# Optimization experiments

Hardware: AMD Instinct MI355X
Metric: run time of the kernel (lower is better)

## Reference

```python
import jax, jax.numpy as jnp
import numpy as np

DIM = 8
EPS = 1e-6
TRIL = DIM * (DIM + 1) // 2  # 36


def _build_L(params):
    # params: [N, TRIL] -> lower-triangular L: [N, DIM, DIM] with diag clamped >= 1e-4
    rows, cols = jnp.tril_indices(DIM)
    L = jnp.zeros((params.shape[0], DIM, DIM), params.dtype)
    L = L.at[:, rows, cols].set(params)
    idx = jnp.arange(DIM)
    d = jnp.clip(L[:, idx, idx], 0.0001)
    return L.at[:, idx, idx].set(d)


def _compute_density(L):
    # L: [N, DIM, DIM] -> PSD trace-1 density matrices [N, DIM, DIM]
    I = jnp.eye(DIM, dtype=L.dtype)
    rho = jnp.einsum('nij,nkj->nik', L, L) + EPS * I
    w = jnp.linalg.eigvalsh(rho)                      # [N, DIM]
    corr = jnp.maximum(-w.min(axis=-1), 0.0) + 1e-6   # shift to PSD
    rho = rho + corr[:, None, None] * I
    tr = jnp.trace(rho, axis1=1, axis2=2)
    return rho / (tr[:, None, None] + EPS)


def _matrix_sqrt(x):
    U, S, Vh = jnp.linalg.svd(x, full_matrices=False)
    sqrt_S = jnp.sqrt(S + EPS)
    return (U * sqrt_S[..., None, :]) @ Vh


def _quantum_fidelity(rho, sigma):
    sqrt_rho = _matrix_sqrt(rho)
    product = sqrt_rho @ sigma @ sqrt_rho
    S = jnp.linalg.svd(product, compute_uv=False)
    f = jnp.sum(jnp.sqrt(S + EPS), axis=-1)
    return jnp.clip(f, 0.0, 1.0)


def setup_inputs() -> dict:
    key = jax.random.key(0)
    k1, k2, k3 = jax.random.split(key, 3)
    B, S, V = 16384, 10, 100000
    contexts = jax.random.randint(k1, (B, S), 0, V)
    targets = jax.random.randint(k2, (B,), 0, V)
    # embedding table, init roughly like the torch module (uniform + diag ramp)
    emb_weight = jax.random.uniform(k3, (V, TRIL), jnp.float32, -0.1, 0.1)
    diag_idx = np.array([i * (i + 1) // 2 + i for i in range(DIM)])
    diag_vals = jnp.linspace(0.1, 1.0, DIM, dtype=jnp.float32)
    emb_weight = emb_weight.at[:, diag_idx].set(jnp.broadcast_to(diag_vals, (V, DIM)))
    return {"contexts": contexts, "targets": targets, "emb_weight": emb_weight}


def reference(contexts, targets, emb_weight):
    B, S = contexts.shape
    # context density matrices
    ctx_params = jnp.take(emb_weight, contexts.reshape(-1), axis=0)   # [B*S, TRIL]
    rho_ctx = _compute_density(_build_L(ctx_params)).reshape(B, S, DIM, DIM)
    mask = (contexts != 0).astype(rho_ctx.dtype)[:, :, None, None]
    context_rho = (rho_ctx * mask).sum(axis=1) / mask.sum(axis=1)     # [B, DIM, DIM]
    # target density matrices
    tgt_params = jnp.take(emb_weight, targets, axis=0)                # [B, TRIL]
    rho_tgt = _compute_density(_build_L(tgt_params))                  # [B, DIM, DIM]
    f = _quantum_fidelity(context_rho, rho_tgt)                       # [B]
    return -jnp.log(jnp.clip(f, 1e-8))
```

## Files before the change

kernel.cpp:

```cpp
#include <hip/hip_runtime.h>
#include <math.h>

#define NB   16384
#define SEQ  10
#define DIM  8
#define TRIL 36

__device__ __forceinline__ constexpr int tri(int r, int c) { return r * (r + 1) / 2 + c; }

template <int CTRL>
__device__ __forceinline__ float fperm(float v) {
    return __int_as_float(__builtin_amdgcn_mov_dpp(__float_as_int(v), CTRL, 0xf, 0xf, true));
}
template <int CTRL>
__device__ __forceinline__ double dperm(double v) {
    long long u = __double_as_longlong(v);
    int lo = (int)(u & 0xffffffffLL);
    int hi = (int)(((unsigned long long)u) >> 32);
    lo = __builtin_amdgcn_mov_dpp(lo, CTRL, 0xf, 0xf, true);
    hi = __builtin_amdgcn_mov_dpp(hi, CTRL, 0xf, 0xf, true);
    return __longlong_as_double(((long long)hi << 32) | (long long)(unsigned)lo);
}
__device__ __forceinline__ float fswz4(float v) {
    return __int_as_float(__builtin_amdgcn_ds_swizzle(__float_as_int(v), 0x101F));
}
__device__ __forceinline__ double dswz4(double v) {
    long long u = __double_as_longlong(v);
    int lo = (int)(u & 0xffffffffLL);
    int hi = (int)(((unsigned long long)u) >> 32);
    lo = __builtin_amdgcn_ds_swizzle(lo, 0x101F);
    hi = __builtin_amdgcn_ds_swizzle(hi, 0x101F);
    return __longlong_as_double(((long long)hi << 32) | (long long)(unsigned)lo);
}

__device__ __forceinline__ double rsqrt1(double x) {
    double r = __builtin_amdgcn_rsq(x);
    return r * (1.5 - 0.5 * x * r * r);
}
__device__ __forceinline__ double rcp1(double x) {
    double r = __builtin_amdgcn_rcp(x);
    return r * (2.0 - x * r);
}
__device__ __forceinline__ double sqrt1(double x) { return x * rsqrt1(x); }

__device__ __forceinline__ void load_row(const float* __restrict__ emb, int tok, float (&F)[TRIL]) {
    const float4* q = (const float4*)(emb + (size_t)tok * TRIL);
    #pragma unroll
    for (int i = 0; i < 9; ++i) {
        float4 v = q[i];
        F[4*i+0] = v.x; F[4*i+1] = v.y; F[4*i+2] = v.z; F[4*i+3] = v.w;
    }
}

template <bool ACCUM>
__device__ __forceinline__ void density_from(float (&Lf)[TRIL], double (&dst)[TRIL]) {
    #pragma unroll
    for (int d = 0; d < DIM; ++d) Lf[tri(d, d)] = fmaxf(Lf[tri(d, d)], 1.0e-4f);
    double tr = 1.6e-5;
    #pragma unroll
    for (int i = 0; i < TRIL; ++i) { double v = (double)Lf[i]; tr += v * v; }
    double inv = rcp1(tr + 1.0e-6);
    #pragma unroll
    for (int i = 0; i < DIM; ++i) {
        #pragma unroll
        for (int j = 0; j <= i; ++j) {
            double sum = (i == j) ? 2.0e-6 : 0.0;
            #pragma unroll
            for (int k = 0; k <= j; ++k) sum += (double)Lf[tri(i, k)] * (double)Lf[tri(j, k)];
            if (ACCUM) dst[tri(i, j)] += sum * inv;
            else       dst[tri(i, j)]  = sum * inv;
        }
    }
}

__device__ __forceinline__ void chol36(double (&M)[TRIL]) {
    #pragma unroll
    for (int j = 0; j < DIM; ++j) {
        double d = M[tri(j, j)];
        #pragma unroll
        for (int k = 0; k < j; ++k) d -= M[tri(j, k)] * M[tri(j, k)];
        d = fmax(d, 1.0e-30);
        double invd = rsqrt1(d);
        M[tri(j, j)] = d * invd;
        #pragma unroll
        for (int i = j + 1; i < DIM; ++i) {
            double v = M[tri(i, j)];
            #pragma unroll
            for (int k = 0; k < j; ++k) v -= M[tri(i, k)] * M[tri(j, k)];
            M[tri(i, j)] = v * invd;
        }
    }
}

template <int M>
__device__ __forceinline__ float jrecv(float v) {
    if constexpr (M == 1) return fperm<0xB1>(v);
    else if constexpr (M == 2) return fperm<0x4E>(v);
    else if constexpr (M == 3) return fperm<0x1B>(v);
    else return __int_as_float(__builtin_amdgcn_ds_swizzle(__float_as_int(v), (M << 10) | 0x1F));
}
template <int M>
__device__ __forceinline__ void jround(float (&o)[DIM], bool& conv) {
    float r[DIM];
    #pragma unroll
    for (int k = 0; k < DIM; ++k) r[k] = jrecv<M>(o[k]);
    float xo = 0.0f, xr = 0.0f, z = 0.0f;
    #pragma unroll
    for (int k = 0; k < DIM; ++k) {
        xo = fmaf(o[k], o[k], xo);
        xr = fmaf(r[k], r[k], xr);
        z  = fmaf(o[k], r[k], z);
    }
    float z2 = z * z;
    float d  = xr - xo;
    if (z2 > 1.0e-12f * xo * xr && z2 > 1.0e-12f * d * d) conv = false;
    if (z2 > 1.0e-16f * xo * xr) {
        float tau = d * (0.5f * __builtin_amdgcn_rcpf(z));
        float t = __builtin_amdgcn_rcpf(fabsf(tau) + sqrtf(fmaf(tau, tau, 1.0f)));
        t = (tau >= 0.0f) ? t : -t;
        float c = __builtin_amdgcn_rsqf(fmaf(t, t, 1.0f));
        float s = t * c;
        #pragma unroll
        for (int k = 0; k < DIM; ++k) o[k] = fmaf(c, o[k], -s * r[k]);
    }
}

__global__ void __launch_bounds__(256, 2)
qcbow_kernel(const int* __restrict__ contexts,
             const int* __restrict__ targets,
             const float* __restrict__ emb,
             float* __restrict__ out)
{
    const int tid = blockIdx.x * 256 + threadIdx.x;
    const int b = tid >> 3;
    const int h = threadIdx.x & 7;
    const bool q0 = (h < 4);

    const int base = b * SEQ;
    int tok1 = contexts[base + h];
    int tok2 = 0;
    if (h < 2)  tok2 = contexts[base + 8 + h];
    if (h >= 4) tok2 = targets[b];

    float F1[TRIL], F2[TRIL];
    load_row(emb, tok1, F1);
    load_row(emb, tok2, F2);

    double A[TRIL];
    #pragma unroll
    for (int i = 0; i < TRIL; ++i) A[i] = 0.0;
    float cntf = 0.0f;

    if (tok1 != 0) { density_from<true>(F1, A); cntf = 1.0f; }
    double T[TRIL];
    density_from<false>(F2, T);
    if (h < 2 && tok2 != 0) {
        #pragma unroll
        for (int i = 0; i < TRIL; ++i) A[i] += T[i];
        cntf += 1.0f;
    }

    #pragma unroll
    for (int i = 0; i < TRIL; ++i) A[i] += dperm<0xB1>(A[i]);
    cntf += fperm<0xB1>(cntf);
    #pragma unroll
    for (int i = 0; i < TRIL; ++i) A[i] += dperm<0x4E>(A[i]);
    cntf += fperm<0x4E>(cntf);
    #pragma unroll
    for (int i = 0; i < TRIL; ++i) A[i] += dswz4(A[i]);
    cntf += fswz4(cntf);

    double invc = rcp1((double)cntf);
    #pragma unroll
    for (int i = 0; i < TRIL; ++i) A[i] *= invc;
    #pragma unroll
    for (int d = 0; d < DIM; ++d) A[tri(d, d)] += 1.0e-6;

    double M[TRIL];
    #pragma unroll
    for (int i = 0; i < TRIL; ++i) M[i] = q0 ? A[i] : T[i];
    chol36(M);

    const bool h1 = (h & 1), h2 = (h & 2);
    double w[DIM];
    #pragma unroll
    for (int k = 0; k < DIM; ++k) {
        #define E(J) ((k >= (J)) ? M[tri((k >= (J)) ? k : (J), (J))] : 0.0)
        double o0 = h1 ? E(5) : E(4);
        double o1 = h1 ? E(7) : E(6);
        double own = h2 ? o1 : o0;
        double s0 = h1 ? E(1) : E(0);
        double s1 = h1 ? E(3) : E(2);
        double snd = h2 ? s1 : s0;
        #undef E
        double sw = dswz4(snd);
        w[k] = q0 ? sw : own;
    }

    double Lx[TRIL];
    #pragma unroll
    for (int i = 0; i < TRIL; ++i) Lx[i] = dswz4(M[i]);
    double Lc[TRIL];
    #pragma unroll
    for (int i = 0; i < TRIL; ++i) Lc[i] = q0 ? M[i] : Lx[i];

    float col[DIM];
    #pragma unroll
    for (int i = 0; i < DIM; ++i) {
        double s = 0.0;
        #pragma unroll
        for (int k = i; k < DIM; ++k) s += Lc[tri(k, i)] * w[k];
        col[i] = (float)s;
    }

    for (int sweep = 0; sweep < 8; ++sweep) {
        bool conv = true;
        jround<1>(col, conv);
        jround<2>(col, conv);
        jround<3>(col, conv);
        jround<4>(col, conv);
        jround<5>(col, conv);
        jround<6>(col, conv);
        jround<7>(col, conv);
        if (sweep >= 2 && __all(conv)) break;
    }

    double xn = 0.0;
    #pragma unroll
    for (int k = 0; k < DIM; ++k) xn += (double)col[k] * (double)col[k];
    double fp = sqrt1(xn + 1.0e-6);
    fp += dperm<0xB1>(fp);
    fp += dperm<0x4E>(fp);
    fp += dswz4(fp);
    if (h == 0) {
        double f = fmin(fp, 1.0);
        f = fmax(f, 1.0e-8);
        out[b] = (float)(-log(f));
    }
}

extern "C" void kernel_launch(void* const* d_in, const int* in_sizes, int n_in,
                              void* d_out, int out_size, void* d_ws, size_t ws_size,
                              hipStream_t stream) {
    const int*   contexts = (const int*)d_in[0];
    const int*   targets  = (const int*)d_in[1];
    const float* emb      = (const float*)d_in[2];
    float*       out      = (float*)d_out;

    qcbow_kernel<<<dim3(NB * 8 / 256), dim3(256), 0, stream>>>(contexts, targets, emb, out);
}
```

Baseline: 87.69 us.

## Replace ds_swizzle lane exchanges with DPP row moves and track Jacobi norms

Every ds_swizzle cross-lane exchange (xor-4 within 8-lane groups) becomes a DPP row_half_mirror (0x141), composed with quad permutes for the Jacobi partner rounds. This removes LDS-path swizzle latency and waitcnts from the reductions and the one-sided Jacobi loop. The Jacobi column norm is now carried as a register and updated analytically after each rotation, so only the partner's norm is exchanged and the self-dot product is not recomputed. Tree-shaped partial sums also shorten dependency chains. The cost is possible float drift from the incrementally updated norm, plus the mirror mapping, which needed the send-index selection to be reordered.

```diff
diff --git a/kernel.cpp b/kernel.cpp
--- a/kernel.cpp
+++ b/kernel.cpp
@@ -21,17 +21,6 @@
     hi = __builtin_amdgcn_mov_dpp(hi, CTRL, 0xf, 0xf, true);
     return __longlong_as_double(((long long)hi << 32) | (long long)(unsigned)lo);
 }
-__device__ __forceinline__ float fswz4(float v) {
-    return __int_as_float(__builtin_amdgcn_ds_swizzle(__float_as_int(v), 0x101F));
-}
-__device__ __forceinline__ double dswz4(double v) {
-    long long u = __double_as_longlong(v);
-    int lo = (int)(u & 0xffffffffLL);
-    int hi = (int)(((unsigned long long)u) >> 32);
-    lo = __builtin_amdgcn_ds_swizzle(lo, 0x101F);
-    hi = __builtin_amdgcn_ds_swizzle(hi, 0x101F);
-    return __longlong_as_double(((long long)hi << 32) | (long long)(unsigned)lo);
-}
 
 __device__ __forceinline__ double rsqrt1(double x) {
     double r = __builtin_amdgcn_rsq(x);
@@ -56,9 +45,14 @@
 __device__ __forceinline__ void density_from(float (&Lf)[TRIL], double (&dst)[TRIL]) {
     #pragma unroll
     for (int d = 0; d < DIM; ++d) Lf[tri(d, d)] = fmaxf(Lf[tri(d, d)], 1.0e-4f);
-    double tr = 1.6e-5;
-    #pragma unroll
-    for (int i = 0; i < TRIL; ++i) { double v = (double)Lf[i]; tr += v * v; }
+    double t0 = 0.0, t1 = 0.0, t2 = 0.0, t3 = 0.0;
+    #pragma unroll
+    for (int i = 0; i < 36; i += 4) {
+        double v0 = (double)Lf[i],   v1 = (double)Lf[i+1];
+        double v2 = (double)Lf[i+2], v3 = (double)Lf[i+3];
+        t0 += v0 * v0; t1 += v1 * v1; t2 += v2 * v2; t3 += v3 * v3;
+    }
+    double tr = ((t0 + t1) + (t2 + t3)) + 1.6e-5;
     double inv = rcp1(tr + 1.0e-6);
     #pragma unroll
     for (int i = 0; i < DIM; ++i) {
@@ -97,20 +91,23 @@
     if constexpr (M == 1) return fperm<0xB1>(v);
     else if constexpr (M == 2) return fperm<0x4E>(v);
     else if constexpr (M == 3) return fperm<0x1B>(v);
-    else return __int_as_float(__builtin_amdgcn_ds_swizzle(__float_as_int(v), (M << 10) | 0x1F));
-}
+    else if constexpr (M == 7) return fperm<0x141>(v);
+    else if constexpr (M == 4) return fperm<0x141>(fperm<0x1B>(v));
+    else if constexpr (M == 5) return fperm<0x141>(fperm<0x4E>(v));
+    else                       return fperm<0x141>(fperm<0xB1>(v));
+}
+
 template <int M>
-__device__ __forceinline__ void jround(float (&o)[DIM], bool& conv) {
+__device__ __forceinline__ void jround(float (&o)[DIM], float& xo, bool& conv) {
     float r[DIM];
     #pragma unroll
     for (int k = 0; k < DIM; ++k) r[k] = jrecv<M>(o[k]);
-    float xo = 0.0f, xr = 0.0f, z = 0.0f;
-    #pragma unroll
-    for (int k = 0; k < DIM; ++k) {
-        xo = fmaf(o[k], o[k], xo);
-        xr = fmaf(r[k], r[k], xr);
-        z  = fmaf(o[k], r[k], z);
-    }
+    float xr = jrecv<M>(xo);
+    float p0 = fmaf(o[1], r[1], o[0] * r[0]);
+    float p1 = fmaf(o[3], r[3], o[2] * r[2]);
+    float p2 = fmaf(o[5], r[5], o[4] * r[4]);
+    float p3 = fmaf(o[7], r[7], o[6] * r[6]);
+    float z  = (p0 + p1) + (p2 + p3);
     float z2 = z * z;
     float d  = xr - xo;
     if (z2 > 1.0e-12f * xo * xr && z2 > 1.0e-12f * d * d) conv = false;
@@ -122,6 +119,8 @@
         float s = t * c;
         #pragma unroll
         for (int k = 0; k < DIM; ++k) o[k] = fmaf(c, o[k], -s * r[k]);
+        float cc = c * c, ss = s * s, cs2 = 2.0f * c * s;
+        xo = fmaf(cc, xo, fmaf(ss, xr, -cs2 * z));
     }
 }
 
@@ -167,8 +166,8 @@
     for (int i = 0; i < TRIL; ++i) A[i] += dperm<0x4E>(A[i]);
     cntf += fperm<0x4E>(cntf);
     #pragma unroll
-    for (int i = 0; i < TRIL; ++i) A[i] += dswz4(A[i]);
-    cntf += fswz4(cntf);
+    for (int i = 0; i < TRIL; ++i) A[i] += dperm<0x141>(A[i]);
+    cntf += fperm<0x141>(cntf);
 
     double invc = rcp1((double)cntf);
     #pragma unroll
@@ -189,17 +188,17 @@
         double o0 = h1 ? E(5) : E(4);
         double o1 = h1 ? E(7) : E(6);
         double own = h2 ? o1 : o0;
-        double s0 = h1 ? E(1) : E(0);
-        double s1 = h1 ? E(3) : E(2);
+        double s0 = h1 ? E(2) : E(3);
+        double s1 = h1 ? E(0) : E(1);
         double snd = h2 ? s1 : s0;
         #undef E
-        double sw = dswz4(snd);
+        double sw = dperm<0x141>(snd);
         w[k] = q0 ? sw : own;
     }
 
     double Lx[TRIL];
     #pragma unroll
-    for (int i = 0; i < TRIL; ++i) Lx[i] = dswz4(M[i]);
+    for (int i = 0; i < TRIL; ++i) Lx[i] = dperm<0x141>(M[i]);
     double Lc[TRIL];
     #pragma unroll
     for (int i = 0; i < TRIL; ++i) Lc[i] = q0 ? M[i] : Lx[i];
@@ -213,15 +212,20 @@
         col[i] = (float)s;
     }
 
+    float q0n = fmaf(col[1], col[1], col[0] * col[0]);
+    float q1n = fmaf(col[3], col[3], col[2] * col[2]);
+    float q2n = fmaf(col[5], col[5], col[4] * col[4]);
+    float q3n = fmaf(col[7], col[7], col[6] * col[6]);
+    float xo = (q0n + q1n) + (q2n + q3n);
     for (int sweep = 0; sweep < 8; ++sweep) {
         bool conv = true;
-        jround<1>(col, conv);
-        jround<2>(col, conv);
-        jround<3>(col, conv);
-        jround<4>(col, conv);
-        jround<5>(col, conv);
-        jround<6>(col, conv);
-        jround<7>(col, conv);
+        jround<1>(col, xo, conv);
+        jround<2>(col, xo, conv);
+        jround<3>(col, xo, conv);
+        jround<4>(col, xo, conv);
+        jround<5>(col, xo, conv);
+        jround<6>(col, xo, conv);
+        jround<7>(col, xo, conv);
         if (sweep >= 2 && __all(conv)) break;
     }
 
@@ -231,7 +235,7 @@
     double fp = sqrt1(xn + 1.0e-6);
     fp += dperm<0xB1>(fp);
     fp += dperm<0x4E>(fp);
-    fp += dswz4(fp);
+    fp += dperm<0x141>(fp);
     if (h == 0) {
         double f = fmin(fp, 1.0);
         f = fmax(f, 1.0e-8);
```

Measured after the change: 87.32 us. About the same (-0.4%).
